# Kernel optimization log

Hardware: AMD Instinct MI355X
Metric: run time of the kernel (lower is better)

Reference implementation:

```python
import jax, jax.numpy as jnp
import numpy as np

NUM_BINS = 4
SCALE = 5.0
EPS = 1e-12

def hswish(x):
    return x * jnp.clip(x + 3.0, 0.0, 6.0) / 6.0

def l2norm(x, axis):
    n = jnp.sqrt(jnp.sum(x * x, axis=axis, keepdims=True))
    return x / jnp.maximum(n, EPS)

def setup_inputs() -> dict:
    key = jax.random.key(0)
    k0, k1, k2, k3, k4 = jax.random.split(key, 5)
    B, C, T, H, W = 8, 256, 32, 28, 28
    hidden, embd = 512, 32
    x = jax.random.normal(k0, (B, C, T, H, W), dtype=jnp.float32)
    W1 = jax.random.normal(k1, (hidden, C), dtype=jnp.float32) * (1.0 / np.sqrt(C))
    b1 = jax.random.normal(k2, (hidden,), dtype=jnp.float32) * 0.01
    W2 = jax.random.normal(k3, (embd, hidden), dtype=jnp.float32) * (1.0 / np.sqrt(hidden))
    b2 = jax.random.normal(k4, (embd,), dtype=jnp.float32) * 0.01
    return {"x": x, "W1": W1, "b1": b1, "W2": W2, "b2": b2}

def reference(x, W1, b1, W2, b2):
    B, C, T, H, W = x.shape
    # encoder: global spatial avg-pool -> 1x1x1 conv -> HSwish -> 1x1x1 conv
    pooled = jnp.mean(x, axis=(3, 4))                      # (B,C,T)
    h = hswish(jnp.einsum('hc,bct->bht', W1, pooled) + b1[None, :, None])
    embds = jnp.einsum('eh,bht->bet', W2, h) + b2[None, :, None]   # (B,E,T)
    norm_embd = l2norm(embds, axis=1)

    # --- grouping (no-grad in original) ---
    ns = jnp.sum(norm_embd[:, :, 1:] * norm_embd[:, :, :-1], axis=1)    # (B,T-1)
    # k-th smallest neighbour similarity = threshold
    smallest = -jax.lax.top_k(-ns, NUM_BINS - 1)[0]                      # ascending smallest k
    threshold = smallest[:, -1]
    edges = (ns > threshold[:, None]).astype(jnp.int32)                  # (B,T-1)
    interval_ends = jnp.concatenate(
        [jnp.zeros((B, 1), dtype=jnp.int32), 1 - edges], axis=1)        # (B,T)
    groups = jnp.cumsum(interval_ends, axis=1)                           # (B,T)
    group_ids = jnp.arange(NUM_BINS, dtype=groups.dtype)
    group_mask = (groups[:, :, None] == group_ids[None, None, :]).astype(jnp.float32)  # (B,T,K)
    group_sizes = jnp.sum(group_mask, axis=1, keepdims=True)             # (B,1,K)
    centers_sum = jnp.einsum('bet,btk->bek', norm_embd, group_mask)      # (B,E,K)
    norm_centers = l2norm(centers_sum / group_sizes, axis=1)             # (B,E,K)
    norm_centers = jax.lax.stop_gradient(norm_centers)

    similarities = jnp.einsum('bet,bek->btk', norm_embd, norm_centers)   # (B,T,K)
    weights = jax.nn.softmax(SCALE * similarities, axis=2)               # (B,T,K)
    sum_weights = jnp.sum(weights, axis=1, keepdims=True)                # (B,1,K)
    scales = jnp.where(sum_weights > 0.0, 1.0 / sum_weights, jnp.ones_like(sum_weights))
    scales = jax.lax.stop_gradient(scales)
    norm_weights = scales * weights                                      # (B,T,K)

    # weighted temporal pooling: avoids (B,C,T,K,H,W) blowup
    out = jnp.einsum('bcthw,btk->bckhw', x, norm_weights)                # (B,C,K,H,W)
    return out
```

## Files before the change

kernel.cpp:

```cpp
#include <hip/hip_runtime.h>
#include <math.h>

#define BATCH 8
#define CCH   256
#define TT    32
#define HWSZ  784
#define HID   512
#define EMB   32
#define KBINS 4
#define SCALEF 5.0f
#define EPSN  1e-12f

__global__ __launch_bounds__(1024) void mlp_kernel(
        const float* __restrict__ x,
        const float* __restrict__ W1, const float* __restrict__ b1,
        const float* __restrict__ W2, const float* __restrict__ b2,
        float* __restrict__ embds) {
    __shared__ float pcol[CCH];
    __shared__ float hcol[HID];

    const int b = blockIdx.x >> 5;
    const int t = blockIdx.x & 31;
    const int tid  = threadIdx.x;
    const int wave = tid >> 6;
    const int lane = tid & 63;

    for (int c = wave; c < CCH; c += 16) {
        const float4* xp = (const float4*)(x + ((size_t)((b * CCH + c) * TT + t)) * HWSZ);
        float s = 0.f;
        for (int f = lane; f < 196; f += 64) {
            float4 v = xp[f];
            s += v.x + v.y + v.z + v.w;
        }
#pragma unroll
        for (int off = 32; off > 0; off >>= 1) s += __shfl_down(s, off);
        if (lane == 0) pcol[c] = s * (1.0f / 784.0f);
    }
    __syncthreads();

    if (tid < HID) {
        const float4* w = (const float4*)(W1 + (size_t)tid * CCH);
        float acc = 0.f;
#pragma unroll 8
        for (int j = 0; j < CCH / 4; j++) {
            float4 wv = w[j];
            acc += wv.x * pcol[4 * j] + wv.y * pcol[4 * j + 1]
                 + wv.z * pcol[4 * j + 2] + wv.w * pcol[4 * j + 3];
        }
        acc += b1[tid];
        float r = fminf(fmaxf(acc + 3.0f, 0.0f), 6.0f);
        hcol[tid] = acc * r * (1.0f / 6.0f);
    }
    __syncthreads();

    {
        const int e = tid >> 5;
        const int l = tid & 31;
        const float* w = W2 + (size_t)e * HID;
        float acc = 0.f;
#pragma unroll
        for (int j = 0; j < HID / 32; j++) acc += w[l + 32 * j] * hcol[l + 32 * j];
        acc += __shfl_down(acc, 16);
        acc += __shfl_down(acc, 8);
        acc += __shfl_down(acc, 4);
        acc += __shfl_down(acc, 2);
        acc += __shfl_down(acc, 1);
        if (l == 0) embds[((size_t)b * EMB + e) * TT + t] = acc + b2[e];
    }
}

__global__ void group_kernel(const float* __restrict__ embds, float* __restrict__ nw) {
    __shared__ float se[EMB][TT + 1];
    __shared__ float ns[TT];
    __shared__ float colinv[TT];
    __shared__ float thr_sh;
    __shared__ float cs[EMB][KBINS];
    __shared__ float wts[TT][KBINS];
    __shared__ float gsize[KBINS];
    __shared__ float kfac[KBINS];
    __shared__ int   gid[TT];

    const int b   = blockIdx.x;
    const int tid = threadIdx.x;

    for (int i = tid; i < EMB * TT; i += 256)
        se[i >> 5][i & 31] = embds[(size_t)b * EMB * TT + i];
    __syncthreads();

    if (tid < TT) {
        float s = 0.f;
        for (int e = 0; e < EMB; e++) { float v = se[e][tid]; s += v * v; }
        colinv[tid] = 1.0f / fmaxf(sqrtf(s), EPSN);
    }
    __syncthreads();
    for (int i = tid; i < EMB * TT; i += 256) {
        int e = i >> 5, t = i & 31;
        se[e][t] *= colinv[t];
    }
    __syncthreads();

    if (tid < TT - 1) {
        float s = 0.f;
        for (int e = 0; e < EMB; e++) s += se[e][tid] * se[e][tid + 1];
        ns[tid] = s;
    }
    __syncthreads();

    if (tid < TT - 1) {
        float v = ns[tid];
        int pos = 0;
        for (int j = 0; j < TT - 1; j++) {
            float u = ns[j];
            pos += (u < v) || (u == v && j < tid);
        }
        if (pos == KBINS - 2) thr_sh = v;
    }
    __syncthreads();

    if (tid < TT) {
        float thr = thr_sh;
        int g = 0;
        for (int s = 1; s <= tid; s++) g += !(ns[s - 1] > thr);
        gid[tid] = g;
    }
    __syncthreads();
    if (tid < KBINS) {
        float c = 0.f;
        for (int t = 0; t < TT; t++) c += (gid[t] == tid);
        gsize[tid] = c;
    }
    __syncthreads();

    if (tid < EMB * KBINS) {
        int e = tid >> 2, k = tid & 3;
        float s = 0.f;
        for (int t = 0; t < TT; t++) if (gid[t] == k) s += se[e][t];
        cs[e][k] = s / gsize[k];
    }
    __syncthreads();
    if (tid < KBINS) {
        float s = 0.f;
        for (int e = 0; e < EMB; e++) { float v = cs[e][tid]; s += v * v; }
        kfac[tid] = 1.0f / fmaxf(sqrtf(s), EPSN);
    }
    __syncthreads();
    if (tid < EMB * KBINS) {
        int e = tid >> 2, k = tid & 3;
        cs[e][k] *= kfac[k];
    }
    __syncthreads();

    if (tid < TT * KBINS) {
        int t = tid >> 2, k = tid & 3;
        float s = 0.f;
        for (int e = 0; e < EMB; e++) s += se[e][t] * cs[e][k];
        wts[t][k] = s * SCALEF;
    }
    __syncthreads();
    if (tid < TT) {
        float m = wts[tid][0];
        for (int k = 1; k < KBINS; k++) m = fmaxf(m, wts[tid][k]);
        float ex[KBINS]; float sum = 0.f;
        for (int k = 0; k < KBINS; k++) { ex[k] = expf(wts[tid][k] - m); sum += ex[k]; }
        float inv = 1.0f / sum;
        for (int k = 0; k < KBINS; k++) wts[tid][k] = ex[k] * inv;
    }
    __syncthreads();
    if (tid < KBINS) {
        float s = 0.f;
        for (int t = 0; t < TT; t++) s += wts[t][tid];
        kfac[tid] = (s > 0.f) ? (1.0f / s) : 1.0f;
    }
    __syncthreads();
    if (tid < TT * KBINS) {
        int t = tid >> 2, k = tid & 3;
        nw[((size_t)b * TT + t) * KBINS + k] = wts[t][k] * kfac[k];
    }
}

__global__ __launch_bounds__(128) void out_kernel(
        const float* __restrict__ x, const float* __restrict__ nw,
        float* __restrict__ out) {
    __shared__ float w[TT * KBINS];
    const int b = blockIdx.x / 392;
    const unsigned idx = (blockIdx.x % 392) * 128 + threadIdx.x;
    w[threadIdx.x] = nw[(size_t)b * TT * KBINS + threadIdx.x];
    __syncthreads();
    const unsigned c = idx / 196;
    const unsigned f = idx % 196;
    const float4* xp = (const float4*)(x + ((size_t)(b * CCH + c) * TT) * HWSZ);
    float4 acc[KBINS];
#pragma unroll
    for (int k = 0; k < KBINS; k++) { acc[k].x = 0.f; acc[k].y = 0.f; acc[k].z = 0.f; acc[k].w = 0.f; }
#pragma unroll 8
    for (int t = 0; t < TT; t++) {
        float4 v = xp[t * 196 + f];
#pragma unroll
        for (int k = 0; k < KBINS; k++) {
            float wk = w[t * KBINS + k];
            acc[k].x += v.x * wk;
            acc[k].y += v.y * wk;
            acc[k].z += v.z * wk;
            acc[k].w += v.w * wk;
        }
    }
    float4* op = (float4*)(out + ((size_t)(b * CCH + c) * KBINS) * HWSZ);
#pragma unroll
    for (int k = 0; k < KBINS; k++) op[k * 196 + f] = acc[k];
}

extern "C" void kernel_launch(void* const* d_in, const int* in_sizes, int n_in,
                              void* d_out, int out_size, void* d_ws, size_t ws_size,
                              hipStream_t stream) {
    const float* x  = (const float*)d_in[0];
    const float* W1 = (const float*)d_in[1];
    const float* b1 = (const float*)d_in[2];
    const float* W2 = (const float*)d_in[3];
    const float* b2 = (const float*)d_in[4];
    float* out = (float*)d_out;

    float* ws    = (float*)d_ws;
    float* embds = ws;
    float* nw    = embds + BATCH * EMB * TT;

    mlp_kernel<<<BATCH * TT, 1024, 0, stream>>>(x, W1, b1, W2, b2, embds);
    group_kernel<<<BATCH, 256, 0, stream>>>(embds, nw);
    out_kernel<<<BATCH * 392, 128, 0, stream>>>(x, nw, out);
}
```

Measured before the change: 345.4 us.

## Fuse MLP, grouping and weighted pooling into one cooperative kernel

Merges the three kernels into a single cooperative launch of 256 blocks of 1024 threads, using grid-wide syncs between the encoder, grouping and output phases. The goal is to remove two kernel launch gaps and the serial tail of the tiny 8-block grouping kernel. The output phase now runs with only 256 large blocks, each thread doing up to two tasks, which may lower memory-level parallelism compared with the former 3136 small blocks. Grid syncs add their own cost, and the grouping phase still leaves most blocks idle while it runs.

```diff
diff --git a/kernel.cpp b/kernel.cpp
--- a/kernel.cpp
+++ b/kernel.cpp
@@ -1,5 +1,8 @@
 #include <hip/hip_runtime.h>
+#include <hip/hip_cooperative_groups.h>
 #include <math.h>
+
+namespace cg = cooperative_groups;
 
 #define BATCH 8
 #define CCH   256
@@ -11,65 +14,19 @@
 #define SCALEF 5.0f
 #define EPSN  1e-12f
 
-__global__ __launch_bounds__(1024) void mlp_kernel(
+#define NTASK  (BATCH * CCH * 196)
+#define NTHREADS (256 * 1024)
+
+__global__ __launch_bounds__(1024) void fused_kernel(
         const float* __restrict__ x,
         const float* __restrict__ W1, const float* __restrict__ b1,
         const float* __restrict__ W2, const float* __restrict__ b2,
-        float* __restrict__ embds) {
+        float* __restrict__ embds, float* __restrict__ nw,
+        float* __restrict__ out) {
+    cg::grid_group grid = cg::this_grid();
+
     __shared__ float pcol[CCH];
     __shared__ float hcol[HID];
-
-    const int b = blockIdx.x >> 5;
-    const int t = blockIdx.x & 31;
-    const int tid  = threadIdx.x;
-    const int wave = tid >> 6;
-    const int lane = tid & 63;
-
-    for (int c = wave; c < CCH; c += 16) {
-        const float4* xp = (const float4*)(x + ((size_t)((b * CCH + c) * TT + t)) * HWSZ);
-        float s = 0.f;
-        for (int f = lane; f < 196; f += 64) {
-            float4 v = xp[f];
-            s += v.x + v.y + v.z + v.w;
-        }
-#pragma unroll
-        for (int off = 32; off > 0; off >>= 1) s += __shfl_down(s, off);
-        if (lane == 0) pcol[c] = s * (1.0f / 784.0f);
-    }
-    __syncthreads();
-
-    if (tid < HID) {
-        const float4* w = (const float4*)(W1 + (size_t)tid * CCH);
-        float acc = 0.f;
-#pragma unroll 8
-        for (int j = 0; j < CCH / 4; j++) {
-            float4 wv = w[j];
-            acc += wv.x * pcol[4 * j] + wv.y * pcol[4 * j + 1]
-                 + wv.z * pcol[4 * j + 2] + wv.w * pcol[4 * j + 3];
-        }
-        acc += b1[tid];
-        float r = fminf(fmaxf(acc + 3.0f, 0.0f), 6.0f);
-        hcol[tid] = acc * r * (1.0f / 6.0f);
-    }
-    __syncthreads();
-
-    {
-        const int e = tid >> 5;
-        const int l = tid & 31;
-        const float* w = W2 + (size_t)e * HID;
-        float acc = 0.f;
-#pragma unroll
-        for (int j = 0; j < HID / 32; j++) acc += w[l + 32 * j] * hcol[l + 32 * j];
-        acc += __shfl_down(acc, 16);
-        acc += __shfl_down(acc, 8);
-        acc += __shfl_down(acc, 4);
-        acc += __shfl_down(acc, 2);
-        acc += __shfl_down(acc, 1);
-        if (l == 0) embds[((size_t)b * EMB + e) * TT + t] = acc + b2[e];
-    }
-}
-
-__global__ void group_kernel(const float* __restrict__ embds, float* __restrict__ nw) {
     __shared__ float se[EMB][TT + 1];
     __shared__ float ns[TT];
     __shared__ float colinv[TT];
@@ -79,134 +36,191 @@
     __shared__ float gsize[KBINS];
     __shared__ float kfac[KBINS];
     __shared__ int   gid[TT];
-
-    const int b   = blockIdx.x;
-    const int tid = threadIdx.x;
-
-    for (int i = tid; i < EMB * TT; i += 256)
-        se[i >> 5][i & 31] = embds[(size_t)b * EMB * TT + i];
+    __shared__ float wtab[BATCH * TT * KBINS];
+
+    const int tid  = threadIdx.x;
+    const int wave = tid >> 6;
+    const int lane = tid & 63;
+
+    {
+        const int b = blockIdx.x >> 5;
+        const int t = blockIdx.x & 31;
+
+        for (int c = wave; c < CCH; c += 16) {
+            const float4* xp = (const float4*)(x + ((size_t)((b * CCH + c) * TT + t)) * HWSZ);
+            float s = 0.f;
+            for (int f = lane; f < 196; f += 64) {
+                float4 v = xp[f];
+                s += v.x + v.y + v.z + v.w;
+            }
+#pragma unroll
+            for (int off = 32; off > 0; off >>= 1) s += __shfl_down(s, off);
+            if (lane == 0) pcol[c] = s * (1.0f / 784.0f);
+        }
+        __syncthreads();
+
+        if (tid < HID) {
+            const float4* w = (const float4*)(W1 + (size_t)tid * CCH);
+            float acc = 0.f;
+#pragma unroll 8
+            for (int j = 0; j < CCH / 4; j++) {
+                float4 wv = w[j];
+                acc += wv.x * pcol[4 * j] + wv.y * pcol[4 * j + 1]
+                     + wv.z * pcol[4 * j + 2] + wv.w * pcol[4 * j + 3];
+            }
+            acc += b1[tid];
+            float r = fminf(fmaxf(acc + 3.0f, 0.0f), 6.0f);
+            hcol[tid] = acc * r * (1.0f / 6.0f);
+        }
+        __syncthreads();
+
+        {
+            const int e = tid >> 5;
+            const int l = tid & 31;
+            const float* w = W2 + (size_t)e * HID;
+            float acc = 0.f;
+#pragma unroll
+            for (int j = 0; j < HID / 32; j++) acc += w[l + 32 * j] * hcol[l + 32 * j];
+            acc += __shfl_down(acc, 16);
+            acc += __shfl_down(acc, 8);
+            acc += __shfl_down(acc, 4);
+            acc += __shfl_down(acc, 2);
+            acc += __shfl_down(acc, 1);
+            if (l == 0) embds[((size_t)b * EMB + e) * TT + t] = acc + b2[e];
+        }
+    }
+
+    grid.sync();
+
+    if (blockIdx.x < BATCH) {
+        const int b = blockIdx.x;
+
+        se[tid >> 5][tid & 31] = embds[(size_t)b * EMB * TT + tid];
+        __syncthreads();
+
+        if (tid < TT) {
+            float s = 0.f;
+            for (int e = 0; e < EMB; e++) { float v = se[e][tid]; s += v * v; }
+            colinv[tid] = 1.0f / fmaxf(sqrtf(s), EPSN);
+        }
+        __syncthreads();
+        se[tid >> 5][tid & 31] *= colinv[tid & 31];
+        __syncthreads();
+
+        if (tid < TT - 1) {
+            float s = 0.f;
+            for (int e = 0; e < EMB; e++) s += se[e][tid] * se[e][tid + 1];
+            ns[tid] = s;
+        }
+        __syncthreads();
+
+        if (tid < TT - 1) {
+            float v = ns[tid];
+            int pos = 0;
+            for (int j = 0; j < TT - 1; j++) {
+                float u = ns[j];
+                pos += (u < v) || (u == v && j < tid);
+            }
+            if (pos == KBINS - 2) thr_sh = v;
+        }
+        __syncthreads();
+
+        if (tid < TT) {
+            float thr = thr_sh;
+            int g = 0;
+            for (int s = 1; s <= tid; s++) g += !(ns[s - 1] > thr);
+            gid[tid] = g;
+        }
+        __syncthreads();
+        if (tid < KBINS) {
+            float c = 0.f;
+            for (int t = 0; t < TT; t++) c += (gid[t] == tid);
+            gsize[tid] = c;
+        }
+        __syncthreads();
+
+        if (tid < EMB * KBINS) {
+            int e = tid >> 2, k = tid & 3;
+            float s = 0.f;
+            for (int t = 0; t < TT; t++) if (gid[t] == k) s += se[e][t];
+            cs[e][k] = s / gsize[k];
+        }
+        __syncthreads();
+        if (tid < KBINS) {
+            float s = 0.f;
+            for (int e = 0; e < EMB; e++) { float v = cs[e][tid]; s += v * v; }
+            kfac[tid] = 1.0f / fmaxf(sqrtf(s), EPSN);
+        }
+        __syncthreads();
+        if (tid < EMB * KBINS) {
+            int e = tid >> 2, k = tid & 3;
+            cs[e][k] *= kfac[k];
+        }
+        __syncthreads();
+
+        if (tid < TT * KBINS) {
+            int t = tid >> 2, k = tid & 3;
+            float s = 0.f;
+            for (int e = 0; e < EMB; e++) s += se[e][t] * cs[e][k];
+            wts[t][k] = s * SCALEF;
+        }
+        __syncthreads();
+        if (tid < TT) {
+            float m = wts[tid][0];
+            for (int k = 1; k < KBINS; k++) m = fmaxf(m, wts[tid][k]);
+            float ex[KBINS]; float sum = 0.f;
+            for (int k = 0; k < KBINS; k++) { ex[k] = expf(wts[tid][k] - m); sum += ex[k]; }
+            float inv = 1.0f / sum;
+            for (int k = 0; k < KBINS; k++) wts[tid][k] = ex[k] * inv;
+        }
+        __syncthreads();
+        if (tid < KBINS) {
+            float s = 0.f;
+            for (int t = 0; t < TT; t++) s += wts[t][tid];
+            kfac[tid] = (s > 0.f) ? (1.0f / s) : 1.0f;
+        }
+        __syncthreads();
+        if (tid < TT * KBINS) {
+            int t = tid >> 2, k = tid & 3;
+            nw[((size_t)b * TT + t) * KBINS + k] = wts[t][k] * kfac[k];
+        }
+    }
+
+    grid.sync();
+
+    wtab[tid] = nw[tid];
     __syncthreads();
 
-    if (tid < TT) {
-        float s = 0.f;
-        for (int e = 0; e < EMB; e++) { float v = se[e][tid]; s += v * v; }
-        colinv[tid] = 1.0f / fmaxf(sqrtf(s), EPSN);
+    const unsigned idx0 = blockIdx.x * 1024 + tid;
+#pragma unroll
+    for (int rep = 0; rep < 2; rep++) {
+        unsigned task = idx0 + rep * NTHREADS;
+        if (task >= NTASK) break;
+        const unsigned b = task / (CCH * 196);
+        const unsigned rem = task - b * (CCH * 196);
+        const unsigned c = rem / 196;
+        const unsigned f = rem - c * 196;
+        const float4* xp = (const float4*)(x + ((size_t)(b * CCH + c) * TT) * HWSZ);
+        const float* wrow = &wtab[b * TT * KBINS];
+        float4 acc[KBINS];
+#pragma unroll
+        for (int k = 0; k < KBINS; k++) { acc[k].x = 0.f; acc[k].y = 0.f; acc[k].z = 0.f; acc[k].w = 0.f; }
+#pragma unroll 8
+        for (int t = 0; t < TT; t++) {
+            float4 v = xp[t * 196 + f];
+#pragma unroll
+            for (int k = 0; k < KBINS; k++) {
+                float wk = wrow[t * KBINS + k];
+                acc[k].x += v.x * wk;
+                acc[k].y += v.y * wk;
+                acc[k].z += v.z * wk;
+                acc[k].w += v.w * wk;
+            }
+        }
+        float4* op = (float4*)(out + ((size_t)(b * CCH + c) * KBINS) * HWSZ);
+#pragma unroll
+        for (int k = 0; k < KBINS; k++) op[k * 196 + f] = acc[k];
     }
-    __syncthreads();
-    for (int i = tid; i < EMB * TT; i += 256) {
-        int e = i >> 5, t = i & 31;
-        se[e][t] *= colinv[t];
-    }
-    __syncthreads();
-
-    if (tid < TT - 1) {
-        float s = 0.f;
-        for (int e = 0; e < EMB; e++) s += se[e][tid] * se[e][tid + 1];
-        ns[tid] = s;
-    }
-    __syncthreads();
-
-    if (tid < TT - 1) {
-        float v = ns[tid];
-        int pos = 0;
-        for (int j = 0; j < TT - 1; j++) {
-            float u = ns[j];
-            pos += (u < v) || (u == v && j < tid);
-        }
-        if (pos == KBINS - 2) thr_sh = v;
-    }
-    __syncthreads();
-
-    if (tid < TT) {
-        float thr = thr_sh;
-        int g = 0;
-        for (int s = 1; s <= tid; s++) g += !(ns[s - 1] > thr);
-        gid[tid] = g;
-    }
-    __syncthreads();
-    if (tid < KBINS) {
-        float c = 0.f;
-        for (int t = 0; t < TT; t++) c += (gid[t] == tid);
-        gsize[tid] = c;
-    }
-    __syncthreads();
-
-    if (tid < EMB * KBINS) {
-        int e = tid >> 2, k = tid & 3;
-        float s = 0.f;
-        for (int t = 0; t < TT; t++) if (gid[t] == k) s += se[e][t];
-        cs[e][k] = s / gsize[k];
-    }
-    __syncthreads();
-    if (tid < KBINS) {
-        float s = 0.f;
-        for (int e = 0; e < EMB; e++) { float v = cs[e][tid]; s += v * v; }
-        kfac[tid] = 1.0f / fmaxf(sqrtf(s), EPSN);
-    }
-    __syncthreads();
-    if (tid < EMB * KBINS) {
-        int e = tid >> 2, k = tid & 3;
-        cs[e][k] *= kfac[k];
-    }
-    __syncthreads();
-
-    if (tid < TT * KBINS) {
-        int t = tid >> 2, k = tid & 3;
-        float s = 0.f;
-        for (int e = 0; e < EMB; e++) s += se[e][t] * cs[e][k];
-        wts[t][k] = s * SCALEF;
-    }
-    __syncthreads();
-    if (tid < TT) {
-        float m = wts[tid][0];
-        for (int k = 1; k < KBINS; k++) m = fmaxf(m, wts[tid][k]);
-        float ex[KBINS]; float sum = 0.f;
-        for (int k = 0; k < KBINS; k++) { ex[k] = expf(wts[tid][k] - m); sum += ex[k]; }
-        float inv = 1.0f / sum;
-        for (int k = 0; k < KBINS; k++) wts[tid][k] = ex[k] * inv;
-    }
-    __syncthreads();
-    if (tid < KBINS) {
-        float s = 0.f;
-        for (int t = 0; t < TT; t++) s += wts[t][tid];
-        kfac[tid] = (s > 0.f) ? (1.0f / s) : 1.0f;
-    }
-    __syncthreads();
-    if (tid < TT * KBINS) {
-        int t = tid >> 2, k = tid & 3;
-        nw[((size_t)b * TT + t) * KBINS + k] = wts[t][k] * kfac[k];
-    }
-}
-
-__global__ __launch_bounds__(128) void out_kernel(
-        const float* __restrict__ x, const float* __restrict__ nw,
-        float* __restrict__ out) {
-    __shared__ float w[TT * KBINS];
-    const int b = blockIdx.x / 392;
-    const unsigned idx = (blockIdx.x % 392) * 128 + threadIdx.x;
-    w[threadIdx.x] = nw[(size_t)b * TT * KBINS + threadIdx.x];
-    __syncthreads();
-    const unsigned c = idx / 196;
-    const unsigned f = idx % 196;
-    const float4* xp = (const float4*)(x + ((size_t)(b * CCH + c) * TT) * HWSZ);
-    float4 acc[KBINS];
-#pragma unroll
-    for (int k = 0; k < KBINS; k++) { acc[k].x = 0.f; acc[k].y = 0.f; acc[k].z = 0.f; acc[k].w = 0.f; }
-#pragma unroll 8
-    for (int t = 0; t < TT; t++) {
-        float4 v = xp[t * 196 + f];
-#pragma unroll
-        for (int k = 0; k < KBINS; k++) {
-            float wk = w[t * KBINS + k];
-            acc[k].x += v.x * wk;
-            acc[k].y += v.y * wk;
-            acc[k].z += v.z * wk;
-            acc[k].w += v.w * wk;
-        }
-    }
-    float4* op = (float4*)(out + ((size_t)(b * CCH + c) * KBINS) * HWSZ);
-#pragma unroll
-    for (int k = 0; k < KBINS; k++) op[k * 196 + f] = acc[k];
 }
 
 extern "C" void kernel_launch(void* const* d_in, const int* in_sizes, int n_in,
@@ -223,7 +237,8 @@
     float* embds = ws;
     float* nw    = embds + BATCH * EMB * TT;
 
-    mlp_kernel<<<BATCH * TT, 1024, 0, stream>>>(x, W1, b1, W2, b2, embds);
-    group_kernel<<<BATCH, 256, 0, stream>>>(embds, nw);
-    out_kernel<<<BATCH * 392, 128, 0, stream>>>(x, nw, out);
+    void* args[] = { (void*)&x, (void*)&W1, (void*)&b1, (void*)&W2, (void*)&b2,
+                     (void*)&embds, (void*)&nw, (void*)&out };
+    hipLaunchCooperativeKernel((const void*)fused_kernel,
+                               dim3(BATCH * TT), dim3(1024), args, 0, stream);
 }
```

After: 405.5 us. 1.17x slower.

## Split spatial pooling into a separate highly parallel kernel before the MLP

Applied to the files above, without the earlier changes.

The spatial average pool moves out of the 256-block MLP kernel into its own kernel. That kernel has one wave per (b,c,t) row and launches 16384 blocks, with fully unrolled float4 loads. The MLP then runs as a lighter 512-thread fc kernel that reads the pooled vectors from workspace. This aims to fix the poor parallelism of the original pooling pass, which used only 256 blocks to stream all of x, at the cost of an extra launch and a small workspace round trip.

```diff
diff --git a/kernel.cpp b/kernel.cpp
--- a/kernel.cpp
+++ b/kernel.cpp
@@ -11,41 +11,56 @@
 #define SCALEF 5.0f
 #define EPSN  1e-12f
 
-__global__ __launch_bounds__(1024) void mlp_kernel(
-        const float* __restrict__ x,
+__global__ __launch_bounds__(256) void pool_kernel(
+        const float* __restrict__ x, float* __restrict__ pooled) {
+    const int wave = threadIdx.x >> 6;
+    const int lane = threadIdx.x & 63;
+    const int row  = blockIdx.x * 4 + wave;
+    const float4* xp = (const float4*)(x + (size_t)row * HWSZ);
+
+    float4 v0 = xp[lane];
+    float4 v1 = xp[lane + 64];
+    float4 v2 = xp[lane + 128];
+    float s = v0.x + v0.y + v0.z + v0.w
+            + v1.x + v1.y + v1.z + v1.w
+            + v2.x + v2.y + v2.z + v2.w;
+    if (lane < 4) {
+        float4 v3 = xp[lane + 192];
+        s += v3.x + v3.y + v3.z + v3.w;
+    }
+#pragma unroll
+    for (int off = 32; off > 0; off >>= 1) s += __shfl_down(s, off);
+    if (lane == 0) {
+        const int t = row & 31;
+        const int c = (row >> 5) & 255;
+        const int b = row >> 13;
+        pooled[((size_t)(b * TT + t)) * CCH + c] = s * (1.0f / 784.0f);
+    }
+}
+
+__global__ __launch_bounds__(512) void fc_kernel(
         const float* __restrict__ W1, const float* __restrict__ b1,
         const float* __restrict__ W2, const float* __restrict__ b2,
-        float* __restrict__ embds) {
-    __shared__ float pcol[CCH];
+        const float* __restrict__ pooled, float* __restrict__ embds) {
+    __shared__ float pc[CCH];
     __shared__ float hcol[HID];
 
     const int b = blockIdx.x >> 5;
     const int t = blockIdx.x & 31;
-    const int tid  = threadIdx.x;
-    const int wave = tid >> 6;
-    const int lane = tid & 63;
-
-    for (int c = wave; c < CCH; c += 16) {
-        const float4* xp = (const float4*)(x + ((size_t)((b * CCH + c) * TT + t)) * HWSZ);
-        float s = 0.f;
-        for (int f = lane; f < 196; f += 64) {
-            float4 v = xp[f];
-            s += v.x + v.y + v.z + v.w;
-        }
-#pragma unroll
-        for (int off = 32; off > 0; off >>= 1) s += __shfl_down(s, off);
-        if (lane == 0) pcol[c] = s * (1.0f / 784.0f);
-    }
-    __syncthreads();
-
-    if (tid < HID) {
+    const int tid = threadIdx.x;
+
+    if (tid < CCH / 4)
+        ((float4*)pc)[tid] = ((const float4*)(pooled + ((size_t)(b * TT + t)) * CCH))[tid];
+    __syncthreads();
+
+    {
         const float4* w = (const float4*)(W1 + (size_t)tid * CCH);
         float acc = 0.f;
 #pragma unroll 8
         for (int j = 0; j < CCH / 4; j++) {
             float4 wv = w[j];
-            acc += wv.x * pcol[4 * j] + wv.y * pcol[4 * j + 1]
-                 + wv.z * pcol[4 * j + 2] + wv.w * pcol[4 * j + 3];
+            acc += wv.x * pc[4 * j] + wv.y * pc[4 * j + 1]
+                 + wv.z * pc[4 * j + 2] + wv.w * pc[4 * j + 3];
         }
         acc += b1[tid];
         float r = fminf(fmaxf(acc + 3.0f, 0.0f), 6.0f);
@@ -54,13 +69,12 @@
     __syncthreads();
 
     {
-        const int e = tid >> 5;
-        const int l = tid & 31;
+        const int e = tid >> 4;
+        const int l = tid & 15;
         const float* w = W2 + (size_t)e * HID;
         float acc = 0.f;
 #pragma unroll
-        for (int j = 0; j < HID / 32; j++) acc += w[l + 32 * j] * hcol[l + 32 * j];
-        acc += __shfl_down(acc, 16);
+        for (int j = 0; j < HID / 16; j++) acc += w[l + 16 * j] * hcol[l + 16 * j];
         acc += __shfl_down(acc, 8);
         acc += __shfl_down(acc, 4);
         acc += __shfl_down(acc, 2);
@@ -219,11 +233,13 @@
     const float* b2 = (const float*)d_in[4];
     float* out = (float*)d_out;
 
-    float* ws    = (float*)d_ws;
-    float* embds = ws;
-    float* nw    = embds + BATCH * EMB * TT;
-
-    mlp_kernel<<<BATCH * TT, 1024, 0, stream>>>(x, W1, b1, W2, b2, embds);
+    float* ws     = (float*)d_ws;
+    float* pooled = ws;
+    float* embds  = pooled + BATCH * TT * CCH;
+    float* nw     = embds + BATCH * EMB * TT;
+
+    pool_kernel<<<BATCH * CCH * TT / 4, 256, 0, stream>>>(x, pooled);
+    fc_kernel<<<BATCH * TT, 512, 0, stream>>>(W1, b1, W2, b2, pooled, embds);
     group_kernel<<<BATCH, 256, 0, stream>>>(embds, nw);
     out_kernel<<<BATCH * 392, 128, 0, stream>>>(x, nw, out);
 }
```

New measurement: 344.9 us. Within noise of the previous version (-0.2%).
